# Performance work log

Measured on AMD Instinct MI355X. Metric: run time of the kernel, lower is better.

Reference implementation:

```python
import jax, jax.numpy as jnp
import numpy as np

N = 100000      # number of agents/nodes
T = 512         # number of timesteps (edges has T-1 steps)
E = 1024        # edge_per_t
MU = 0.05       # diffusion rate (init kwarg mu)
RHO = 32.0      # sigmoid sharpness (init kwarg rho)


def setup_inputs() -> dict:
    key = jax.random.key(0)
    k1, k2, k3, k4, k5 = jax.random.split(key, 5)
    logit_X0 = jax.random.normal(k1, (N,), dtype=jnp.float32)
    theta = jax.random.normal(k2, (1,), dtype=jnp.float32)
    u = jax.random.randint(k3, (T - 1, E), 0, N)
    v = jax.random.randint(k4, (T - 1, E), 0, N)
    s = jax.random.randint(k5, (T - 1, E), 0, 2)  # activation flag in {0,1}
    edges = jnp.stack([u, v, s], axis=-1).astype(jnp.int32)  # [T-1, E, 3]
    return {"logit_X0": logit_X0, "theta": theta, "edges": edges}


def reference(logit_X0, theta, edges):
    X0 = jax.nn.sigmoid(logit_X0)          # [N]
    epsilon = jax.nn.sigmoid(theta)         # [1]

    def step(X_t, e):
        # e: [E, 3] -> (u, v, s). Gather-diff-scale-scatter update.
        u, v = e[:, 0], e[:, 1]
        s = e[:, 2].astype(X_t.dtype)
        d = (X_t[u] - X_t[v]) * s           # [E]
        upd = jnp.zeros_like(X_t).at[u].add(-d).at[v].add(d)
        X_next = X_t + MU * upd
        return X_next, X_next

    _, Xs = jax.lax.scan(step, X0, edges)   # Xs: [T-1, N]
    X = jnp.concatenate([X0[None, :], Xs], axis=0)  # [T, N]

    # diff_X = X[t, u] - X[t, v] with t = step index (state before update)
    Xp = X[:-1]                              # [T-1, N]
    diff = (jnp.take_along_axis(Xp, edges[:, :, 0], axis=1)
            - jnp.take_along_axis(Xp, edges[:, :, 1], axis=1))  # [T-1, E]
    kappa = jax.nn.sigmoid(RHO * (epsilon - jnp.abs(diff.reshape(-1))))
    return X, kappa
```

## Files before the change

### kernel.cpp

```cpp
#include <hip/hip_runtime.h>
#include <math.h>

#define NN 100000
#define TT 512
#define EE 1024
#define NSTEP (TT - 1)
#define NE (NSTEP * EE)
#define NCHUNK (NE / 256)
#define FLOWG 512
#define MU 0.05f
#define RHO 32.0f
#define CAP (NE * 2)
#define NOTREADY 0xFFFFFFFFu
#define SCAN_BLK 1024
#define SCAN_NB ((NN + SCAN_BLK - 1) / SCAN_BLK)
#define RB 32
#define NRC (TT / RB)
#define FILL_BX ((NN / 4 + 255) / 256)

#define SYS __HIP_MEMORY_SCOPE_SYSTEM
#define WGS __HIP_MEMORY_SCOPE_WORKGROUP
#define RLX __ATOMIC_RELAXED

__device__ __forceinline__ float sigmoid_f(float x) {
    return 1.0f / (1.0f + expf(-x));
}

__device__ __forceinline__ unsigned try_val(unsigned* pub, int p) {
    return __hip_atomic_load(&pub[p], RLX, SYS);
}
__device__ __forceinline__ void publish(unsigned* pub, int p, float v) {
    __hip_atomic_store(&pub[p], __float_as_uint(v), RLX, SYS);
}

__device__ __forceinline__ int lower_bound(const unsigned* __restrict__ a,
                                           int lo, int hi, unsigned key) {
    while (lo < hi) {
        int mid = (lo + hi) >> 1;
        if (a[mid] < key) lo = mid + 1; else hi = mid;
    }
    return lo;
}

__global__ void k_init(const float* __restrict__ logit, float* __restrict__ X0f,
                       float* __restrict__ out, int* __restrict__ cnt,
                       int* __restrict__ cur) {
    int n = blockIdx.x * blockDim.x + threadIdx.x;
    if (n < NN) {
        float x = sigmoid_f(logit[n]);
        X0f[n] = x;
        out[n] = x;
        cnt[n] = 0;
        cur[n] = 0;
    }
}

__global__ void k_count(const int* __restrict__ edges, int* __restrict__ cnt,
                        unsigned* __restrict__ pub) {
    int i = blockIdx.x * blockDim.x + threadIdx.x;
    if (i < NE) {
        pub[2 * i]     = NOTREADY;
        pub[2 * i + 1] = NOTREADY;
        int s = edges[3 * i + 2];
        if (s) {
            atomicAdd(&cnt[edges[3 * i + 0]], 1);
            atomicAdd(&cnt[edges[3 * i + 1]], 1);
        }
    }
}

__global__ void __launch_bounds__(256) k_scanA(const int* __restrict__ cnt,
                                               int* __restrict__ bsum) {
    __shared__ int sh[256];
    const int t = threadIdx.x;
    const int base = blockIdx.x * SCAN_BLK + t * 4;
    int s = 0;
    if (base + 3 < NN) {
        const int4 v = *(const int4*)(cnt + base);
        s = v.x + v.y + v.z + v.w;
    } else {
        for (int k = 0; k < 4; ++k) if (base + k < NN) s += cnt[base + k];
    }
    sh[t] = s;
    __syncthreads();
    for (int o = 128; o > 0; o >>= 1) {
        if (t < o) sh[t] += sh[t + o];
        __syncthreads();
    }
    if (t == 0) bsum[blockIdx.x] = sh[0];
}

__global__ void __launch_bounds__(128) k_scanB(int* __restrict__ bsum) {
    __shared__ int sh[128];
    const int t = threadIdx.x;
    int v = (t < SCAN_NB) ? bsum[t] : 0;
    sh[t] = v;
    __syncthreads();
    for (int o = 1; o < 128; o <<= 1) {
        int x = (t >= o) ? sh[t - o] : 0;
        __syncthreads();
        sh[t] += x;
        __syncthreads();
    }
    if (t < SCAN_NB) bsum[t] = sh[t] - v;
}

__global__ void __launch_bounds__(256) k_scanC(const int* __restrict__ cnt,
                                               const int* __restrict__ bsum,
                                               int* __restrict__ off) {
    __shared__ int sh[256];
    const int t = threadIdx.x;
    const int base = blockIdx.x * SCAN_BLK + t * 4;
    int a0 = 0, a1 = 0, a2 = 0, a3 = 0;
    if (base + 3 < NN) {
        const int4 v = *(const int4*)(cnt + base);
        a0 = v.x; a1 = v.y; a2 = v.z; a3 = v.w;
    } else {
        if (base + 0 < NN) a0 = cnt[base + 0];
        if (base + 1 < NN) a1 = cnt[base + 1];
        if (base + 2 < NN) a2 = cnt[base + 2];
    }
    const int s = a0 + a1 + a2 + a3;
    sh[t] = s;
    __syncthreads();
    for (int o = 1; o < 256; o <<= 1) {
        int x = (t >= o) ? sh[t - o] : 0;
        __syncthreads();
        sh[t] += x;
        __syncthreads();
    }
    int ex = sh[t] - s + bsum[blockIdx.x];
    if (base + 3 < NN) {
        int4 w; w.x = ex; w.y = ex + a0; w.z = ex + a0 + a1; w.w = ex + a0 + a1 + a2;
        *(int4*)(off + base) = w;
    } else {
        if (base + 0 < NN) off[base + 0] = ex;
        if (base + 1 < NN) off[base + 1] = ex + a0;
        if (base + 2 < NN) off[base + 2] = ex + a0 + a1;
    }
}

__global__ void k_place(const int* __restrict__ edges,
                        const int* __restrict__ off, int* __restrict__ cur,
                        unsigned* __restrict__ ent) {
    int i = blockIdx.x * blockDim.x + threadIdx.x;
    if (i < NE) {
        int s = edges[3 * i + 2];
        if (s) {
            int u = edges[3 * i + 0];
            int v = edges[3 * i + 1];
            unsigned key = ((unsigned)i) << 1;
            ent[off[u] + atomicAdd(&cur[u], 1)] = key;
            ent[off[v] + atomicAdd(&cur[v], 1)] = key | 1u;
        }
    }
}

__global__ void k_sort(const int* __restrict__ off, const int* __restrict__ cur,
                       unsigned* __restrict__ ent) {
    int n = blockIdx.x * blockDim.x + threadIdx.x;
    if (n >= NN) return;
    int lo = off[n], c = cur[n];
    for (int k = 1; k < c; ++k) {
        unsigned key = ent[lo + k];
        int j = k;
        while (j > 0 && ent[lo + j - 1] > key) {
            ent[lo + j] = ent[lo + j - 1];
            --j;
        }
        ent[lo + j] = key;
    }
}

__global__ void __launch_bounds__(256, 2)
k_flow(const int* __restrict__ edges, const float* __restrict__ theta,
       const float* __restrict__ X0f, const int* __restrict__ off,
       const int* __restrict__ cur, const unsigned* __restrict__ ent,
       unsigned* __restrict__ pub, float* __restrict__ out_kappa) {
    const float eps = sigmoid_f(theta[0]);
    for (int c = blockIdx.x; c < NCHUNK; c += gridDim.x) {
        const int i = (c << 8) + threadIdx.x;
        const int t = i >> 10;
        const int u = edges[3 * i + 0];
        const int v = edges[3 * i + 1];
        const int s = edges[3 * i + 2];

        const unsigned stepkey = ((unsigned)t) << 11;

        const int lu = off[u], hu = lu + cur[u];
        const int qu = lower_bound(ent, lu, hu, stepkey);
        const int lv = off[v], hv = lv + cur[v];
        const int qv = lower_bound(ent, lv, hv, stepkey);

        int mu_ = -1, mv_ = -1;
        if (s) {
            const unsigned ku = ((unsigned)i) << 1;
            mu_ = qu; while (ent[mu_] != ku) ++mu_;
            const unsigned kv = ku | 1u;
            mv_ = qv; while (ent[mv_] != kv) ++mv_;
        }

        bool have_xu = (qu == lu);
        bool have_xv = (qv == lv);
        float xu = have_xu ? X0f[u] : 0.0f;
        float xv = have_xv ? X0f[v] : 0.0f;
        bool kap_done = false;
        bool pu_done = (s == 0);
        bool pv_done = (s == 0);
        float m = 0.0f;

        while (!(kap_done && pu_done && pv_done)) {
            if (!have_xu) {
                unsigned w = try_val(pub, qu - 1);
                if (w != NOTREADY) { xu = __uint_as_float(w); have_xu = true; }
            }
            if (!have_xv) {
                unsigned w = try_val(pub, qv - 1);
                if (w != NOTREADY) { xv = __uint_as_float(w); have_xv = true; }
            }
            if (have_xu && have_xv && !kap_done) {
                float diff = xu - xv;
                m = MU * diff;
                out_kappa[i] = sigmoid_f(RHO * (eps - fabsf(diff)));
                kap_done = true;
            }
            if (kap_done && !pu_done) {
                bool rdy; float baseu = xu;
                if (mu_ == qu) rdy = true;
                else {
                    unsigned w = try_val(pub, mu_ - 1);
                    rdy = (w != NOTREADY);
                    if (rdy) baseu = __uint_as_float(w);
                }
                if (rdy) { publish(pub, mu_, baseu - m); pu_done = true; }
            }
            if (kap_done && !pv_done) {
                bool rdy; float basev = xv;
                if (mv_ == qv) rdy = true;
                else {
                    unsigned w = try_val(pub, mv_ - 1);
                    rdy = (w != NOTREADY);
                    if (rdy) basev = __uint_as_float(w);
                }
                if (rdy) { publish(pub, mv_, basev + m); pv_done = true; }
            }
            if (!(kap_done && pu_done && pv_done)) __builtin_amdgcn_s_sleep(1);
        }
    }
}

__global__ void __launch_bounds__(256) k_fill_pub(float* __restrict__ out,
                                                  const float* __restrict__ X0f,
                                                  const int* __restrict__ off,
                                                  const int* __restrict__ cur,
                                                  const unsigned* __restrict__ ent,
                                                  const unsigned* __restrict__ pub) {
    const int n0 = (blockIdx.x * 256 + threadIdx.x) * 4;
    if (n0 >= NN) return;
    const int r0 = blockIdx.y * RB;
    const unsigned key0 = ((unsigned)r0) << 11;

    int   p[4], e2[4];
    unsigned nxt[4];
    float val[4];
    #pragma unroll
    for (int j = 0; j < 4; ++j) {
        const int n = n0 + j;
        const int lo = off[n];
        e2[j] = lo + cur[n];
        int q = lower_bound(ent, lo, e2[j], key0);
        val[j] = (q > lo) ? __uint_as_float(pub[q - 1]) : X0f[n];
        p[j] = q;
        nxt[j] = (q < e2[j]) ? ent[q] : 0xFFFFFFFFu;
    }

    const int rstart = (r0 == 0) ? 1 : r0;
    for (int r = rstart; r < r0 + RB; ++r) {
        const unsigned lim = ((unsigned)r) << 11;
        #pragma unroll
        for (int j = 0; j < 4; ++j) {
            while (nxt[j] < lim) {
                val[j] = __uint_as_float(pub[p[j]]);
                ++p[j];
                nxt[j] = (p[j] < e2[j]) ? ent[p[j]] : 0xFFFFFFFFu;
            }
        }
        float4 w; w.x = val[0]; w.y = val[1]; w.z = val[2]; w.w = val[3];
        *(float4*)(out + (size_t)r * NN + n0) = w;
    }
}

__global__ void __launch_bounds__(1024) k_seq(const int* __restrict__ edges,
                                              const float* __restrict__ theta,
                                              float* __restrict__ X,
                                              float* __restrict__ out_kappa,
                                              float* __restrict__ md) {
    const int tid = threadIdx.x;
    const float eps = sigmoid_f(theta[0]);
    int u = edges[3 * tid + 0];
    int v = edges[3 * tid + 1];
    int s = edges[3 * tid + 2];
    for (int t = 0; t < NSTEP; ++t) {
        int nu = 0, nv = 0, ns = 0;
        if (t + 1 < NSTEP) {
            const int nb = (t + 1) * 3 * EE + 3 * tid;
            nu = edges[nb + 0]; nv = edges[nb + 1]; ns = edges[nb + 2];
        }
        float xu = __hip_atomic_load(&X[u], RLX, WGS);
        float xv = __hip_atomic_load(&X[v], RLX, WGS);
        float diff = xu - xv;
        out_kappa[t * EE + tid] = sigmoid_f(RHO * (eps - fabsf(diff)));
        bool act = (s && diff != 0.0f);
        float m = act ? MU * diff : 0.0f;
        md[t * EE + tid] = m;
        __syncthreads();
        if (act) {
            __hip_atomic_fetch_add(&X[u], -m, RLX, WGS);
            __hip_atomic_fetch_add(&X[v],  m, RLX, WGS);
        }
        __syncthreads();
        u = nu; v = nv; s = ns;
    }
}

__global__ void k_fill_md(float* __restrict__ out,
                          const int* __restrict__ off, const int* __restrict__ cur,
                          const unsigned* __restrict__ ent,
                          const float* __restrict__ md) {
    int n = blockIdx.x * blockDim.x + threadIdx.x;
    if (n >= NN) return;
    float val = out[n];
    int p = off[n];
    const int e2 = p + cur[n];
    unsigned nxt = (p < e2) ? ent[p] : 0xFFFFFFFFu;
    for (int r = 1; r < TT; ++r) {
        const unsigned lim = ((unsigned)r) << 11;
        while (nxt < lim) {
            float m = md[nxt >> 1];
            val += (nxt & 1u) ? m : -m;
            ++p;
            nxt = (p < e2) ? ent[p] : 0xFFFFFFFFu;
        }
        out[(size_t)r * NN + n] = val;
    }
}

extern "C" void kernel_launch(void* const* d_in, const int* in_sizes, int n_in,
                              void* d_out, int out_size, void* d_ws, size_t ws_size,
                              hipStream_t stream) {
    const float* logit = (const float*)d_in[0];
    const float* theta = (const float*)d_in[1];
    const int*   edges = (const int*)d_in[2];
    float* out = (float*)d_out;
    float* kap = out + (size_t)TT * NN;

    char* ws = (char*)d_ws;
    float*    X0f  = (float*)ws;    ws += sizeof(float) * NN;
    int*      cnt  = (int*)ws;      ws += sizeof(int) * NN;
    int*      off  = (int*)ws;      ws += sizeof(int) * NN;
    int*      cur  = (int*)ws;      ws += sizeof(int) * NN;
    int*      bsum = (int*)ws;      ws += sizeof(int) * ((SCAN_NB + 3) & ~3);
    unsigned* ent  = (unsigned*)ws; ws += sizeof(unsigned) * CAP;
    unsigned* pub = (unsigned*)ws;
    float*    md  = (float*)ws;

    const size_t need_main = (size_t)(4 * NN + SCAN_NB + 3) * 4
                           + (size_t)CAP * 4 * 2;
    const bool main_path = ws_size >= need_main;

    k_init <<<(NN + 255) / 256, 256, 0, stream>>>(logit, X0f, out, cnt, cur);
    k_count<<<(NE + 255) / 256, 256, 0, stream>>>(edges, cnt, pub);
    k_scanA<<<SCAN_NB, 256, 0, stream>>>(cnt, bsum);
    k_scanB<<<1, 128, 0, stream>>>(bsum);
    k_scanC<<<SCAN_NB, 256, 0, stream>>>(cnt, bsum, off);
    k_place<<<(NE + 255) / 256, 256, 0, stream>>>(edges, off, cur, ent);
    k_sort <<<(NN + 255) / 256, 256, 0, stream>>>(off, cur, ent);

    bool flow_ok = false;
    if (main_path) {
        const int* a_edges = edges; const float* a_theta = theta;
        const float* a_x0 = X0f; const int* a_off = off; const int* a_cur = cur;
        const unsigned* a_ent = ent; unsigned* a_pub = pub; float* a_kap = kap;
        void* args[] = { &a_edges, &a_theta, &a_x0, &a_off, &a_cur,
                         &a_ent, &a_pub, &a_kap };
        hipError_t e = hipLaunchCooperativeKernel((const void*)k_flow,
                                                  dim3(FLOWG), dim3(256),
                                                  args, 0, stream);
        if (e == hipSuccess) {
            flow_ok = true;
            k_fill_pub<<<dim3(FILL_BX, NRC), 256, 0, stream>>>(out, X0f, off,
                                                               cur, ent, pub);
        } else {
            (void)hipGetLastError();
        }
    }
    if (!flow_ok) {
        k_seq<<<1, 1024, 0, stream>>>(edges, theta, X0f, kap, md);
        k_fill_md<<<(NN + 255) / 256, 256, 0, stream>>>(out, off, cur, ent, md);
    }
}
```

Baseline: 254.2 us.

## Fuse dataflow and fill kernels into one cooperative launch with spin-wait consumers

Merges the dependency-driven flow kernel and the trajectory fill kernel into a single cooperative kernel. The first 512 blocks run the per-edge publish dataflow while the other 512 blocks write the output X rows, spin-waiting on published values, so filling the large output overlaps with the serial dependency chain. Atomic scope is narrowed from system to agent, and the sleep backoff becomes exponential. It also raises the launch-bounds occupancy target and moves the kappa write after the publishes. The risk is that fill blocks polling memory compete with the critical-path blocks for bandwidth and issue slots.

Result: slower. 312.3 us (+22.9%).

```diff
diff --git a/kernel.cpp b/kernel.cpp
--- a/kernel.cpp
+++ b/kernel.cpp
@@ -8,6 +8,7 @@
 #define NE (NSTEP * EE)
 #define NCHUNK (NE / 256)
 #define FLOWG 512
+#define FILLB 512
 #define MU 0.05f
 #define RHO 32.0f
 #define CAP (NE * 2)
@@ -17,8 +18,9 @@
 #define RB 32
 #define NRC (TT / RB)
 #define FILL_BX ((NN / 4 + 255) / 256)
-
-#define SYS __HIP_MEMORY_SCOPE_SYSTEM
+#define NTILE (FILL_BX * NRC)
+
+#define AGT __HIP_MEMORY_SCOPE_AGENT
 #define WGS __HIP_MEMORY_SCOPE_WORKGROUP
 #define RLX __ATOMIC_RELAXED
 
@@ -26,11 +28,23 @@
     return 1.0f / (1.0f + expf(-x));
 }
 
-__device__ __forceinline__ unsigned try_val(unsigned* pub, int p) {
-    return __hip_atomic_load(&pub[p], RLX, SYS);
+__device__ __forceinline__ unsigned try_val(const unsigned* pub, int p) {
+    return __hip_atomic_load((unsigned*)&pub[p], RLX, AGT);
 }
 __device__ __forceinline__ void publish(unsigned* pub, int p, float v) {
-    __hip_atomic_store(&pub[p], __float_as_uint(v), RLX, SYS);
+    __hip_atomic_store(&pub[p], __float_as_uint(v), RLX, AGT);
+}
+__device__ __forceinline__ float spin_val(const unsigned* pub, int p) {
+    unsigned w = try_val(pub, p);
+    int tries = 0;
+    while (w == NOTREADY) {
+        if (tries < 4)       __builtin_amdgcn_s_sleep(1);
+        else if (tries < 16) __builtin_amdgcn_s_sleep(4);
+        else                 __builtin_amdgcn_s_sleep(8);
+        ++tries;
+        w = try_val(pub, p);
+    }
+    return __uint_as_float(w);
 }
 
 __device__ __forceinline__ int lower_bound(const unsigned* __restrict__ a,
@@ -172,121 +186,133 @@
     }
 }
 
-__global__ void __launch_bounds__(256, 2)
-k_flow(const int* __restrict__ edges, const float* __restrict__ theta,
-       const float* __restrict__ X0f, const int* __restrict__ off,
-       const int* __restrict__ cur, const unsigned* __restrict__ ent,
-       unsigned* __restrict__ pub, float* __restrict__ out_kappa) {
-    const float eps = sigmoid_f(theta[0]);
-    for (int c = blockIdx.x; c < NCHUNK; c += gridDim.x) {
-        const int i = (c << 8) + threadIdx.x;
-        const int t = i >> 10;
-        const int u = edges[3 * i + 0];
-        const int v = edges[3 * i + 1];
-        const int s = edges[3 * i + 2];
-
-        const unsigned stepkey = ((unsigned)t) << 11;
-
-        const int lu = off[u], hu = lu + cur[u];
-        const int qu = lower_bound(ent, lu, hu, stepkey);
-        const int lv = off[v], hv = lv + cur[v];
-        const int qv = lower_bound(ent, lv, hv, stepkey);
-
-        int mu_ = -1, mv_ = -1;
-        if (s) {
-            const unsigned ku = ((unsigned)i) << 1;
-            mu_ = qu; while (ent[mu_] != ku) ++mu_;
-            const unsigned kv = ku | 1u;
-            mv_ = qv; while (ent[mv_] != kv) ++mv_;
-        }
-
-        bool have_xu = (qu == lu);
-        bool have_xv = (qv == lv);
-        float xu = have_xu ? X0f[u] : 0.0f;
-        float xv = have_xv ? X0f[v] : 0.0f;
-        bool kap_done = false;
-        bool pu_done = (s == 0);
-        bool pv_done = (s == 0);
-        float m = 0.0f;
-
-        while (!(kap_done && pu_done && pv_done)) {
-            if (!have_xu) {
-                unsigned w = try_val(pub, qu - 1);
-                if (w != NOTREADY) { xu = __uint_as_float(w); have_xu = true; }
+__global__ void __launch_bounds__(256, 4)
+k_combo(const int* __restrict__ edges, const float* __restrict__ theta,
+        const float* __restrict__ X0f, const int* __restrict__ off,
+        const int* __restrict__ cur, const unsigned* __restrict__ ent,
+        unsigned* __restrict__ pub, float* __restrict__ out_kappa,
+        float* __restrict__ out) {
+    const int bid = blockIdx.x;
+    if (bid < FLOWG) {
+        const float eps = sigmoid_f(theta[0]);
+        for (int c = bid; c < NCHUNK; c += FLOWG) {
+            const int i = (c << 8) + threadIdx.x;
+            const int t = i >> 10;
+            const int u = edges[3 * i + 0];
+            const int v = edges[3 * i + 1];
+            const int s = edges[3 * i + 2];
+
+            const unsigned stepkey = ((unsigned)t) << 11;
+
+            const int lu = off[u], hu = lu + cur[u];
+            const int qu = lower_bound(ent, lu, hu, stepkey);
+            const int lv = off[v], hv = lv + cur[v];
+            const int qv = lower_bound(ent, lv, hv, stepkey);
+
+            int mu_ = -1, mv_ = -1;
+            if (s) {
+                const unsigned ku = ((unsigned)i) << 1;
+                mu_ = qu; while (ent[mu_] != ku) ++mu_;
+                const unsigned kv = ku | 1u;
+                mv_ = qv; while (ent[mv_] != kv) ++mv_;
             }
-            if (!have_xv) {
-                unsigned w = try_val(pub, qv - 1);
-                if (w != NOTREADY) { xv = __uint_as_float(w); have_xv = true; }
+
+            bool have_xu = (qu == lu);
+            bool have_xv = (qv == lv);
+            float xu = have_xu ? X0f[u] : 0.0f;
+            float xv = have_xv ? X0f[v] : 0.0f;
+            bool m_rdy = false;
+            bool pu_done = (s == 0);
+            bool pv_done = (s == 0);
+            bool kap_done = false;
+            float m = 0.0f, diff = 0.0f;
+            int tries = 0;
+
+            while (!(pu_done && pv_done && kap_done)) {
+                if (!have_xu) {
+                    unsigned w = try_val(pub, qu - 1);
+                    if (w != NOTREADY) { xu = __uint_as_float(w); have_xu = true; }
+                }
+                if (!have_xv) {
+                    unsigned w = try_val(pub, qv - 1);
+                    if (w != NOTREADY) { xv = __uint_as_float(w); have_xv = true; }
+                }
+                if (have_xu && have_xv && !m_rdy) {
+                    diff = xu - xv;
+                    m = MU * diff;
+                    m_rdy = true;
+                }
+                if (m_rdy && !pu_done) {
+                    if (mu_ == qu) { publish(pub, mu_, xu - m); pu_done = true; }
+                    else {
+                        unsigned w = try_val(pub, mu_ - 1);
+                        if (w != NOTREADY) {
+                            publish(pub, mu_, __uint_as_float(w) - m);
+                            pu_done = true;
+                        }
+                    }
+                }
+                if (m_rdy && !pv_done) {
+                    if (mv_ == qv) { publish(pub, mv_, xv + m); pv_done = true; }
+                    else {
+                        unsigned w = try_val(pub, mv_ - 1);
+                        if (w != NOTREADY) {
+                            publish(pub, mv_, __uint_as_float(w) + m);
+                            pv_done = true;
+                        }
+                    }
+                }
+                if (m_rdy && !kap_done) {
+                    out_kappa[i] = sigmoid_f(RHO * (eps - fabsf(diff)));
+                    kap_done = true;
+                }
+                if (!(pu_done && pv_done && kap_done)) {
+                    if (tries < 4)       __builtin_amdgcn_s_sleep(1);
+                    else if (tries < 16) __builtin_amdgcn_s_sleep(4);
+                    else                 __builtin_amdgcn_s_sleep(8);
+                    ++tries;
+                }
             }
-            if (have_xu && have_xv && !kap_done) {
-                float diff = xu - xv;
-                m = MU * diff;
-                out_kappa[i] = sigmoid_f(RHO * (eps - fabsf(diff)));
-                kap_done = true;
+        }
+    } else {
+        const int f = bid - FLOWG;
+        for (int tau = f; tau < NTILE; tau += FILLB) {
+            const int rc = tau / FILL_BX;
+            const int bx = tau - rc * FILL_BX;
+            const int n0 = (bx * 256 + threadIdx.x) * 4;
+            if (n0 >= NN) continue;
+            const int r0 = rc * RB;
+            const unsigned key0 = ((unsigned)r0) << 11;
+
+            int   p[4], e2[4];
+            unsigned nxt[4];
+            float val[4];
+            #pragma unroll
+            for (int j = 0; j < 4; ++j) {
+                const int n = n0 + j;
+                const int lo = off[n];
+                e2[j] = lo + cur[n];
+                int q = lower_bound(ent, lo, e2[j], key0);
+                val[j] = (q > lo) ? spin_val(pub, q - 1) : X0f[n];
+                p[j] = q;
+                nxt[j] = (q < e2[j]) ? ent[q] : 0xFFFFFFFFu;
             }
-            if (kap_done && !pu_done) {
-                bool rdy; float baseu = xu;
-                if (mu_ == qu) rdy = true;
-                else {
-                    unsigned w = try_val(pub, mu_ - 1);
-                    rdy = (w != NOTREADY);
-                    if (rdy) baseu = __uint_as_float(w);
-                }
-                if (rdy) { publish(pub, mu_, baseu - m); pu_done = true; }
+
+            const int rstart = (r0 == 0) ? 1 : r0;
+            for (int r = rstart; r < r0 + RB; ++r) {
+                const unsigned lim = ((unsigned)r) << 11;
+                #pragma unroll
+                for (int j = 0; j < 4; ++j) {
+                    while (nxt[j] < lim) {
+                        val[j] = spin_val(pub, p[j]);
+                        ++p[j];
+                        nxt[j] = (p[j] < e2[j]) ? ent[p[j]] : 0xFFFFFFFFu;
+                    }
+                }
+                float4 w; w.x = val[0]; w.y = val[1]; w.z = val[2]; w.w = val[3];
+                *(float4*)(out + (size_t)r * NN + n0) = w;
             }
-            if (kap_done && !pv_done) {
-                bool rdy; float basev = xv;
-                if (mv_ == qv) rdy = true;
-                else {
-                    unsigned w = try_val(pub, mv_ - 1);
-                    rdy = (w != NOTREADY);
-                    if (rdy) basev = __uint_as_float(w);
-                }
-                if (rdy) { publish(pub, mv_, basev + m); pv_done = true; }
-            }
-            if (!(kap_done && pu_done && pv_done)) __builtin_amdgcn_s_sleep(1);
-        }
-    }
-}
-
-__global__ void __launch_bounds__(256) k_fill_pub(float* __restrict__ out,
-                                                  const float* __restrict__ X0f,
-                                                  const int* __restrict__ off,
-                                                  const int* __restrict__ cur,
-                                                  const unsigned* __restrict__ ent,
-                                                  const unsigned* __restrict__ pub) {
-    const int n0 = (blockIdx.x * 256 + threadIdx.x) * 4;
-    if (n0 >= NN) return;
-    const int r0 = blockIdx.y * RB;
-    const unsigned key0 = ((unsigned)r0) << 11;
-
-    int   p[4], e2[4];
-    unsigned nxt[4];
-    float val[4];
-    #pragma unroll
-    for (int j = 0; j < 4; ++j) {
-        const int n = n0 + j;
-        const int lo = off[n];
-        e2[j] = lo + cur[n];
-        int q = lower_bound(ent, lo, e2[j], key0);
-        val[j] = (q > lo) ? __uint_as_float(pub[q - 1]) : X0f[n];
-        p[j] = q;
-        nxt[j] = (q < e2[j]) ? ent[q] : 0xFFFFFFFFu;
-    }
-
-    const int rstart = (r0 == 0) ? 1 : r0;
-    for (int r = rstart; r < r0 + RB; ++r) {
-        const unsigned lim = ((unsigned)r) << 11;
-        #pragma unroll
-        for (int j = 0; j < 4; ++j) {
-            while (nxt[j] < lim) {
-                val[j] = __uint_as_float(pub[p[j]]);
-                ++p[j];
-                nxt[j] = (p[j] < e2[j]) ? ent[p[j]] : 0xFFFFFFFFu;
-            }
-        }
-        float4 w; w.x = val[0]; w.y = val[1]; w.z = val[2]; w.w = val[3];
-        *(float4*)(out + (size_t)r * NN + n0) = w;
+        }
     }
 }
 
@@ -381,15 +407,14 @@
         const int* a_edges = edges; const float* a_theta = theta;
         const float* a_x0 = X0f; const int* a_off = off; const int* a_cur = cur;
         const unsigned* a_ent = ent; unsigned* a_pub = pub; float* a_kap = kap;
+        float* a_out = out;
         void* args[] = { &a_edges, &a_theta, &a_x0, &a_off, &a_cur,
-                         &a_ent, &a_pub, &a_kap };
-        hipError_t e = hipLaunchCooperativeKernel((const void*)k_flow,
-                                                  dim3(FLOWG), dim3(256),
+                         &a_ent, &a_pub, &a_kap, &a_out };
+        hipError_t e = hipLaunchCooperativeKernel((const void*)k_combo,
+                                                  dim3(FLOWG + FILLB), dim3(256),
                                                   args, 0, stream);
         if (e == hipSuccess) {
             flow_ok = true;
-            k_fill_pub<<<dim3(FILL_BX, NRC), 256, 0, stream>>>(out, X0f, off,
-                                                               cur, ent, pub);
         } else {
             (void)hipGetLastError();
         }
```
